# Kernel tuning notes

Measured on AMD Instinct MI355X. Metric: run time of the kernel, lower is better.

Reference implementation:

```python
import jax, jax.numpy as jnp
import numpy as np

B, N, C = 2, 2048, 1024
H = 8                 # num_heads
WS = 256              # window_size; half-window = WS // 2
D = C // H            # head_dim


def setup_inputs() -> dict:
    key = jax.random.key(0)
    k0, k1, k2 = jax.random.split(key, 3)
    s = 0.02  # init scale for weights
    x = jax.random.normal(k0, (B, N, C), dtype=jnp.float32)
    w_qkv = jax.random.normal(k1, (3 * C, C), dtype=jnp.float32) * s
    b_qkv = jnp.zeros((3 * C,), dtype=jnp.float32)
    w_proj = jax.random.normal(k2, (C, C), dtype=jnp.float32) * s
    b_proj = jnp.zeros((C,), dtype=jnp.float32)
    return {"x": x, "w_qkv": w_qkv, "b_qkv": b_qkv, "w_proj": w_proj, "b_proj": b_proj}


def reference(x, w_qkv, b_qkv, w_proj, b_proj):
    b, n, c = x.shape
    # qkv projection (torch Linear: x @ W^T + b) -> (B, N, 3C)
    qkv = x @ w_qkv.T + b_qkv
    # (B, N, 3, H, D) -> (3, B, H, N, D)
    qkv = qkv.reshape(b, n, 3, H, D).transpose(2, 0, 3, 1, 4)
    q, k, v = qkv[0], qkv[1], qkv[2]
    # dense scores over sequence, scaled by sqrt(full dim C) as in the source
    attn = jnp.einsum('bhqd,bhkd->bhqk', q, k) / jnp.sqrt(jnp.asarray(c, x.dtype))
    # banded (local-window) mask: keep |i - j| < WS // 2
    i = jnp.arange(n)[:, None]
    j = jnp.arange(n)[None, :]
    band = jnp.abs(i - j) < (WS // 2)
    attn = jnp.where(band, attn, -jnp.inf)
    attn = jax.nn.softmax(attn, axis=-1)
    out = jnp.einsum('bhqk,bhkd->bhqd', attn, v)     # (B, H, N, D)
    out = out.transpose(0, 2, 1, 3).reshape(b, n, c)  # merge heads
    return out @ w_proj.T + b_proj
```

## Files before the change

kernel.cpp:

```cpp
#include <hip/hip_runtime.h>
#include <hip/hip_bf16.h>
#include <stdint.h>

typedef __hip_bfloat16 bf16;
typedef __attribute__((ext_vector_type(8))) short short8;
typedef __attribute__((ext_vector_type(4))) float floatx4;

#define MFMA_BF16(a, b, c) __builtin_amdgcn_mfma_f32_16x16x32_bf16((a), (b), (c), 0, 0, 0)


__device__ __forceinline__ void gl_lds16(const bf16* gsrc, bf16* lds_dst)
{
    __builtin_amdgcn_global_load_lds(
        (const __attribute__((address_space(1))) uint32_t*)(uintptr_t)gsrc,
        (__attribute__((address_space(3))) uint32_t*)(uintptr_t)lds_dst,
        16, 0, 0);
}

__device__ __forceinline__ int sniff_bf16(const uint16_t* __restrict__ x)
{
    int cnt = 0;
#pragma unroll
    for (int i = 0; i < 64; ++i) {
        const int e = (x[2 * i] >> 7) & 0xFF;
        cnt += (e >= 100 && e <= 140) ? 1 : 0;
    }
    return (cnt >= 32) ? 1 : 0;
}

__global__ void __launch_bounds__(256)
cvt_all_kernel(const void* __restrict__ x, const void* __restrict__ wq,
               const void* __restrict__ wp, const void* __restrict__ bq,
               const void* __restrict__ bp,
               bf16* __restrict__ xb, bf16* __restrict__ wqb,
               bf16* __restrict__ wpb, float* __restrict__ bqf,
               float* __restrict__ bpf)
{
    __shared__ int sflag;
    if (threadIdx.x == 0) sflag = sniff_bf16((const uint16_t*)x);
    __syncthreads();
    const bool isbf = (sflag != 0);

    const int blk = blockIdx.x;
    if (blk < 4096) {
        const void* src; bf16* dst; int base;
        if (blk < 2048)      { src = x;  dst = xb;  base = blk << 11; }
        else if (blk < 3584) { src = wq; dst = wqb; base = (blk - 2048) << 11; }
        else                 { src = wp; dst = wpb; base = (blk - 3584) << 11; }
        const int i = base + (int)threadIdx.x * 8;
        if (isbf) {
            *(uint4*)(dst + i) = *(const uint4*)((const bf16*)src + i);
        } else {
            const float4 f0 = *(const float4*)((const float*)src + i);
            const float4 f1 = *(const float4*)((const float*)src + i + 4);
            bf16 o[8];
            o[0] = __float2bfloat16(f0.x); o[1] = __float2bfloat16(f0.y);
            o[2] = __float2bfloat16(f0.z); o[3] = __float2bfloat16(f0.w);
            o[4] = __float2bfloat16(f1.x); o[5] = __float2bfloat16(f1.y);
            o[6] = __float2bfloat16(f1.z); o[7] = __float2bfloat16(f1.w);
            *(uint4*)(dst + i) = *(uint4*)o;
        }
    } else {
        const void* src; float* dst; int base, n;
        if (blk < 4099) { src = bq; dst = bqf; base = (blk - 4096) * 1024; n = 3072; }
        else            { src = bp; dst = bpf; base = 0;                   n = 1024; }
        const int i0 = base + (int)threadIdx.x * 4;
#pragma unroll
        for (int k = 0; k < 4; ++k) {
            const int idx = i0 + k;
            if (idx < n)
                dst[idx] = isbf ? __bfloat162float(((const bf16*)src)[idx])
                                : ((const float*)src)[idx];
        }
    }
}

template <bool FUSE_VT, bool DYN_OUT>
__global__ void __launch_bounds__(256, 2)
gemm_bt_kernel(const bf16* __restrict__ A, const bf16* __restrict__ W,
               const float* __restrict__ bias, void* __restrict__ Cout,
               int M, int Nc, int K, bf16* __restrict__ Vt,
               const uint16_t* __restrict__ sniffsrc)
{
    __shared__ __align__(16) bf16 As[2][128][32];
    __shared__ __align__(16) bf16 Bs[2][128][32];
    __shared__ int sflag;

    const int tid  = threadIdx.x;
    const int lane = tid & 63;
    const int wave = tid >> 6;
    const int quad = lane >> 4;
    const int l16  = lane & 15;
    const int wm   = (wave & 1) * 64;
    const int wn   = (wave >> 1) * 64;
    const int bm   = blockIdx.x * 128;
    const int bn   = blockIdx.y * 128;

    if (DYN_OUT && tid == 0) sflag = sniff_bf16(sniffsrc);

    const int grow = wave * 32 + (lane >> 2);
    const int gcol = (lane & 3) * 8;
    const bf16* Ag = A + (size_t)(bm + grow) * K + gcol;
    const bf16* Wg = W + (size_t)(bn + grow) * K + gcol;
    bf16* Asb = &As[0][0][0];
    bf16* Bsb = &Bs[0][0][0];
    const int w0 = (wave * 2 + 0) * 512;
    const int w1 = (wave * 2 + 1) * 512;

    floatx4 acc[4][4];
#pragma unroll
    for (int i = 0; i < 4; ++i)
#pragma unroll
        for (int j = 0; j < 4; ++j)
#pragma unroll
            for (int r = 0; r < 4; ++r) acc[i][j][r] = 0.0f;

    for (int k0 = 0; k0 < K; k0 += 64) {
        gl_lds16(Ag + k0,                       Asb + w0);
        gl_lds16(Ag + (size_t)16 * K + k0,      Asb + w1);
        gl_lds16(Ag + k0 + 32,                  Asb + 4096 + w0);
        gl_lds16(Ag + (size_t)16 * K + k0 + 32, Asb + 4096 + w1);
        gl_lds16(Wg + k0,                       Bsb + w0);
        gl_lds16(Wg + (size_t)16 * K + k0,      Bsb + w1);
        gl_lds16(Wg + k0 + 32,                  Bsb + 4096 + w0);
        gl_lds16(Wg + (size_t)16 * K + k0 + 32, Bsb + 4096 + w1);
        __syncthreads();

#pragma unroll
        for (int ks = 0; ks < 2; ++ks) {
            short8 af[4], bfr[4];
#pragma unroll
            for (int i = 0; i < 4; ++i)
                af[i] = *(const short8*)(&As[ks][wm + i * 16 + l16][quad * 8]);
#pragma unroll
            for (int j = 0; j < 4; ++j)
                bfr[j] = *(const short8*)(&Bs[ks][wn + j * 16 + l16][quad * 8]);
#pragma unroll
            for (int i = 0; i < 4; ++i)
#pragma unroll
                for (int j = 0; j < 4; ++j)
                    acc[i][j] = MFMA_BF16(af[i], bfr[j], acc[i][j]);
        }
        __syncthreads();
    }

    const bool outbf = DYN_OUT ? (sflag != 0) : true;

#pragma unroll
    for (int i = 0; i < 4; ++i) {
#pragma unroll
        for (int j = 0; j < 4; ++j) {
            const int col = bn + wn + j * 16 + l16;
            const float bv = bias[col];
#pragma unroll
            for (int r = 0; r < 4; ++r) {
                const int row = bm + wm + i * 16 + quad * 4 + r;
                const float v = acc[i][j][r] + bv;
                const size_t idx = (size_t)row * Nc + col;
                if (!DYN_OUT || outbf) {
                    ((bf16*)Cout)[idx] = __float2bfloat16(v);
                } else {
                    ((float*)Cout)[idx] = v;
                }
                if (FUSE_VT) {
                    if (col >= 2048) {
                        const int hh = (col - 2048) >> 7;
                        const int dd = (col - 2048) & 127;
                        const int bb = row >> 11;
                        const int nn = row & 2047;
                        Vt[(((size_t)bb * 8 + hh) * 128 + dd) * 2048 + nn] =
                            __float2bfloat16(v);
                    }
                }
            }
        }
    }
}

__global__ void __launch_bounds__(64, 4)
attn_kernel(const bf16* __restrict__ qkv, const bf16* __restrict__ Vt,
            bf16* __restrict__ out)
{
    const int lane = threadIdx.x & 63;
    const int quad = lane >> 4;
    const int l16  = lane & 15;

    const int hb = blockIdx.x & 15;
    const int qw = blockIdx.x >> 4;
    const int h  = hb & 7;
    const int b  = hb >> 3;
    const int q0 = qw * 16;

    short8 qf[4];
    {
        const bf16* Qbase = qkv + (size_t)(b * 2048 + q0 + l16) * 3072 + h * 128 + quad * 8;
#pragma unroll
        for (int d = 0; d < 4; ++d)
            qf[d] = *(const short8*)(Qbase + d * 32);
    }

    floatx4 Oacc[8];
#pragma unroll
    for (int dt = 0; dt < 8; ++dt)
#pragma unroll
        for (int r = 0; r < 4; ++r) Oacc[dt][r] = 0.0f;
    float psum[4] = {0.0f, 0.0f, 0.0f, 0.0f};

    __shared__ __align__(16) bf16 Plds[2][16][72];

    int lo = q0 - 127; if (lo < 0) lo = 0; lo &= ~63;
    int hi = q0 + 15 + 127; if (hi > 2047) hi = 2047;

    const bf16* Kb0 = qkv + (size_t)b * 2048 * 3072 + 1024 + h * 128 + quad * 8;
    const bf16* Vb0 = Vt + ((size_t)(b * 8 + h) * 128) * 2048;

    int t = 0;
    for (int key0 = lo; key0 <= hi; key0 += 64, ++t) {
        floatx4 s[4];
#pragma unroll
        for (int qt = 0; qt < 4; ++qt) {
#pragma unroll
            for (int r = 0; r < 4; ++r) s[qt][r] = 0.0f;
            const bf16* Kb = Kb0 + (size_t)(key0 + qt * 16 + l16) * 3072;
#pragma unroll
            for (int d = 0; d < 4; ++d) {
                short8 kf = *(const short8*)(Kb + d * 32);
                s[qt] = MFMA_BF16(qf[d], kf, s[qt]);
            }
        }
#pragma unroll
        for (int qt = 0; qt < 4; ++qt) {
#pragma unroll
            for (int r = 0; r < 4; ++r) {
                const int i = q0 + quad * 4 + r;
                const int j = key0 + qt * 16 + l16;
                const bool ok = (unsigned)(i - j + 127) < 255u;
                const float p = ok ? __expf(s[qt][r] * 0.03125f) : 0.0f;
                psum[r] += p;
                Plds[t & 1][quad * 4 + r][qt * 16 + l16] = __float2bfloat16(p);
            }
        }
#pragma unroll
        for (int ks = 0; ks < 2; ++ks) {
            short8 pf = *(const short8*)(&Plds[t & 1][l16][ks * 32 + quad * 8]);
            const bf16* Vb = Vb0 + key0 + ks * 32 + quad * 8;
#pragma unroll
            for (int dt = 0; dt < 8; ++dt) {
                short8 vf = *(const short8*)(Vb + (size_t)(dt * 16 + l16) * 2048);
                Oacc[dt] = MFMA_BF16(pf, vf, Oacc[dt]);
            }
        }
    }

#pragma unroll
    for (int m = 1; m <= 8; m <<= 1)
#pragma unroll
        for (int r = 0; r < 4; ++r)
            psum[r] += __shfl_xor(psum[r], m, 64);

#pragma unroll
    for (int r = 0; r < 4; ++r) {
        const float inv = 1.0f / psum[r];
        const int row = q0 + quad * 4 + r;
#pragma unroll
        for (int dt = 0; dt < 8; ++dt) {
            out[(size_t)(b * 2048 + row) * 1024 + h * 128 + dt * 16 + l16] =
                __float2bfloat16(Oacc[dt][r] * inv);
        }
    }
}

extern "C" void kernel_launch(void* const* d_in, const int* in_sizes, int n_in,
                              void* d_out, int out_size, void* d_ws, size_t ws_size,
                              hipStream_t stream)
{
    (void)in_sizes; (void)n_in; (void)out_size; (void)ws_size;

    const void* x      = d_in[0];
    const void* w_qkv  = d_in[1];
    const void* b_qkv  = d_in[2];
    const void* w_proj = d_in[3];
    const void* b_proj = d_in[4];

    char* ws = (char*)d_ws;
    bf16*  qkv      = (bf16*)(ws);
    bf16*  Vt       = (bf16*)(ws + 25165824);
    bf16*  attn_out = (bf16*)(ws + 33554432);
    bf16*  xb       = (bf16*)(ws + 41943040);
    bf16*  wqkvb    = (bf16*)(ws + 50331648);
    bf16*  wprojb   = (bf16*)(ws + 56623104);
    float* bqf      = (float*)(ws + 58720256);
    float* bpf      = (float*)(ws + 58732544);

    cvt_all_kernel<<<dim3(4100), dim3(256), 0, stream>>>(
        x, w_qkv, w_proj, b_qkv, b_proj, xb, wqkvb, wprojb, bqf, bpf);

    gemm_bt_kernel<true, false><<<dim3(32, 24), dim3(256), 0, stream>>>(
        xb, wqkvb, bqf, qkv, 4096, 3072, 1024, Vt, (const uint16_t*)x);

    attn_kernel<<<dim3(2048), dim3(64), 0, stream>>>(qkv, Vt, attn_out);

    gemm_bt_kernel<false, true><<<dim3(32, 8), dim3(256), 0, stream>>>(
        attn_out, wprojb, bpf, d_out, 4096, 1024, 1024, nullptr, (const uint16_t*)x);
}
```

Baseline: 188.0 us.

## Share K/V tiles across four waves via LDS in attention kernel

The attention kernel goes from one 16-query wave per block to four waves covering 64 queries. Each 64-key K and V tile is staged into shared memory once with global_load_lds and read by all four waves, instead of every wave fetching it from global memory. This removes redundant global traffic but adds two block barriers per key step and spreads the union key range over all waves, so each wave does some extra masked work.

```diff
diff --git a/kernel.cpp b/kernel.cpp
--- a/kernel.cpp
+++ b/kernel.cpp
@@ -177,19 +177,25 @@
     }
 }
 
-__global__ void __launch_bounds__(64, 4)
+__global__ void __launch_bounds__(256, 2)
 attn_kernel(const bf16* __restrict__ qkv, const bf16* __restrict__ Vt,
             bf16* __restrict__ out)
 {
-    const int lane = threadIdx.x & 63;
+    __shared__ __align__(16) bf16 Kl[16 * 512];
+    __shared__ __align__(16) bf16 Vl[16 * 512];
+    __shared__ __align__(16) bf16 Plds[2][4][16][72];
+
+    const int tid  = threadIdx.x;
+    const int wave = tid >> 6;
+    const int lane = tid & 63;
     const int quad = lane >> 4;
     const int l16  = lane & 15;
 
     const int hb = blockIdx.x & 15;
-    const int qw = blockIdx.x >> 4;
+    const int qb = blockIdx.x >> 4;
     const int h  = hb & 7;
     const int b  = hb >> 3;
-    const int q0 = qw * 16;
+    const int q0 = qb * 64 + wave * 16;
 
     short8 qf[4];
     {
@@ -206,47 +212,62 @@
         for (int r = 0; r < 4; ++r) Oacc[dt][r] = 0.0f;
     float psum[4] = {0.0f, 0.0f, 0.0f, 0.0f};
 
-    __shared__ __align__(16) bf16 Plds[2][16][72];
-
-    int lo = q0 - 127; if (lo < 0) lo = 0; lo &= ~63;
-    int hi = q0 + 15 + 127; if (hi > 2047) hi = 2047;
-
-    const bf16* Kb0 = qkv + (size_t)b * 2048 * 3072 + 1024 + h * 128 + quad * 8;
-    const bf16* Vb0 = Vt + ((size_t)(b * 8 + h) * 128) * 2048;
+    const int sl = lane & 15;
+    const int sq = lane >> 4;
+    const bf16* Kbase = qkv + (size_t)b * 2048 * 3072 + 1024 + h * 128;
+    const bf16* Vtb   = Vt + (size_t)hb * 128 * 2048;
+
+    int lo = qb * 64 - 127; if (lo < 0) lo = 0; lo &= ~63;
+    int hi = qb * 64 + 63 + 127; if (hi > 2047) hi = 2047;
 
     int t = 0;
     for (int key0 = lo; key0 <= hi; key0 += 64, ++t) {
+        __syncthreads();
+#pragma unroll
+        for (int i = 0; i < 4; ++i) {
+            const int tk = wave * 4 + i;
+            const int kt = tk >> 2, dc = tk & 3;
+            gl_lds16(Kbase + (size_t)(key0 + kt * 16 + sl) * 3072 + dc * 32 + sq * 8,
+                     Kl + tk * 512);
+        }
+#pragma unroll
+        for (int i = 0; i < 4; ++i) {
+            const int tv = wave * 4 + i;
+            const int dt = tv >> 1, ks = tv & 1;
+            gl_lds16(Vtb + (size_t)(dt * 16 + sl) * 2048 + key0 + ks * 32 + sq * 8,
+                     Vl + tv * 512);
+        }
+        __syncthreads();
+
         floatx4 s[4];
 #pragma unroll
-        for (int qt = 0; qt < 4; ++qt) {
-#pragma unroll
-            for (int r = 0; r < 4; ++r) s[qt][r] = 0.0f;
-            const bf16* Kb = Kb0 + (size_t)(key0 + qt * 16 + l16) * 3072;
-#pragma unroll
-            for (int d = 0; d < 4; ++d) {
-                short8 kf = *(const short8*)(Kb + d * 32);
-                s[qt] = MFMA_BF16(qf[d], kf, s[qt]);
+        for (int kt = 0; kt < 4; ++kt) {
+#pragma unroll
+            for (int r = 0; r < 4; ++r) s[kt][r] = 0.0f;
+#pragma unroll
+            for (int dc = 0; dc < 4; ++dc) {
+                short8 kf = *(const short8*)(Kl + (kt * 4 + dc) * 512 + lane * 8);
+                s[kt] = MFMA_BF16(qf[dc], kf, s[kt]);
             }
         }
 #pragma unroll
-        for (int qt = 0; qt < 4; ++qt) {
+        for (int kt = 0; kt < 4; ++kt) {
 #pragma unroll
             for (int r = 0; r < 4; ++r) {
                 const int i = q0 + quad * 4 + r;
-                const int j = key0 + qt * 16 + l16;
+                const int j = key0 + kt * 16 + l16;
                 const bool ok = (unsigned)(i - j + 127) < 255u;
-                const float p = ok ? __expf(s[qt][r] * 0.03125f) : 0.0f;
+                const float p = ok ? __expf(s[kt][r] * 0.03125f) : 0.0f;
                 psum[r] += p;
-                Plds[t & 1][quad * 4 + r][qt * 16 + l16] = __float2bfloat16(p);
+                Plds[t & 1][wave][quad * 4 + r][kt * 16 + l16] = __float2bfloat16(p);
             }
         }
 #pragma unroll
         for (int ks = 0; ks < 2; ++ks) {
-            short8 pf = *(const short8*)(&Plds[t & 1][l16][ks * 32 + quad * 8]);
-            const bf16* Vb = Vb0 + key0 + ks * 32 + quad * 8;
+            short8 pf = *(const short8*)(&Plds[t & 1][wave][l16][ks * 32 + quad * 8]);
 #pragma unroll
             for (int dt = 0; dt < 8; ++dt) {
-                short8 vf = *(const short8*)(Vb + (size_t)(dt * 16 + l16) * 2048);
+                short8 vf = *(const short8*)(Vl + (dt * 2 + ks) * 512 + lane * 8);
                 Oacc[dt] = MFMA_BF16(pf, vf, Oacc[dt]);
             }
         }
@@ -298,7 +319,7 @@
     gemm_bt_kernel<true, false><<<dim3(32, 24), dim3(256), 0, stream>>>(
         xb, wqkvb, bqf, qkv, 4096, 3072, 1024, Vt, (const uint16_t*)x);
 
-    attn_kernel<<<dim3(2048), dim3(64), 0, stream>>>(qkv, Vt, attn_out);
+    attn_kernel<<<dim3(512), dim3(256), 0, stream>>>(qkv, Vt, attn_out);
 
     gemm_bt_kernel<false, true><<<dim3(32, 8), dim3(256), 0, stream>>>(
         attn_out, wprojb, bpf, d_out, 4096, 1024, 1024, nullptr, (const uint16_t*)x);
```

Result: faster. 162.1 us (-13.8%).
